# Kernel tuning notes

Measured on AMD Instinct MI355X. Metric: run time of the kernel, lower is better.

## Reference

```python
import jax, jax.numpy as jnp
import numpy as np

THRESH = 0.1  # Hardshrink lambda from init_kwargs


def setup_inputs() -> dict:
    key = jax.random.key(0)
    k1, k2, k3 = jax.random.split(key, 3)
    m, n, N = 64, 256, 131072
    phi = jax.random.normal(k1, (m, n), dtype=jnp.float32)
    X = jax.random.normal(k2, (n, N), dtype=jnp.float32)
    Y = jax.random.normal(k3, (m, N), dtype=jnp.float32)
    step = jnp.ones((1,), dtype=jnp.float32)  # learnable ISTA step size
    return {"phi": phi, "X": X, "Y": Y, "step": step, "idx": 100000}


def reference(phi, X, Y, step, idx):
    # The torch module updates column idx, then columns 0..idx-1, each with
    #   X[:, i] = hardshrink(X[:, i] + step * phi.T @ (Y[:, i] - phi @ X[:, i]))
    # (note: -(-1)*step == +step). Columns are independent and each column
    # reads only its own pre-update value, so the per-column loop is exactly
    # equivalent to two batched GEMMs over the prefix X[:, :idx+1] plus one
    # fused hard-threshold pass.
    k = idx + 1  # number of updated columns (idx is a static Python int)
    cols = X[:, :k]                       # [n, k]
    resid = Y[:, :k] - phi @ cols         # [m, k]
    upd = cols + step[0] * (phi.T @ resid)  # [n, k] gradient step
    upd = jnp.where(jnp.abs(upd) > THRESH, upd, jnp.zeros((), upd.dtype))
    X = X.at[:, :k].set(upd)
    return phi, X
```

## Files before the change

### kernel.cpp

```cpp
#include <hip/hip_runtime.h>
#include <math.h>

constexpr int M   = 64;
constexpr int NR  = 256;
constexpr int KK  = NR + M;
constexpr int NC  = 131072;
constexpr int BN  = 64;
constexpr float THR = 0.1f;

typedef __bf16 bf16x8 __attribute__((ext_vector_type(8)));
typedef float  f32x4  __attribute__((ext_vector_type(4)));

static __device__ __forceinline__ unsigned short f2bf(float f) {
    unsigned int u = __float_as_uint(f);
    u += 0x7FFFu + ((u >> 16) & 1u);
    return (unsigned short)(u >> 16);
}

__global__ __launch_bounds__(256)
void k_copy_phi(const float* __restrict__ phi, float* __restrict__ out)
{
    int i = blockIdx.x * 256 + threadIdx.x;
    out[i] = phi[i];
}

__global__ __launch_bounds__(256)
void k_prep(const float* __restrict__ phi, const float* __restrict__ step,
            unsigned short* __restrict__ A)
{
    __shared__ float ph[M * NR];
    const int i = blockIdx.x, j = threadIdx.x;
    for (int t = j; t < M * NR; t += 256) ph[t] = phi[t];
    __syncthreads();
    const float s = step[0];
    float d = 0.f;
    #pragma unroll
    for (int m = 0; m < M; ++m)
        d = fmaf(ph[m * NR + i], ph[m * NR + j], d);
    float w = ((i == j) ? 1.f : 0.f) - s * d;
    A[i * KK + j] = f2bf(w);
    if (j < M) A[i * KK + NR + j] = f2bf(s * ph[j * NR + i]);
}

__global__ __launch_bounds__(256, 3)
void k_gemm(const unsigned short* __restrict__ A,
            const float* __restrict__ X,
            const float* __restrict__ Y,
            const int*   __restrict__ idxp,
            float* __restrict__ outX)
{
    const int k   = idxp[0] + 1;
    const int n0  = blockIdx.x * BN;
    const int tid = threadIdx.x;

    if (n0 >= k) {
        const int c4 = tid & 15, rg = tid >> 4;
        #pragma unroll 4
        for (int r = rg; r < NR; r += 16) {
            const float4* src = (const float4*)(X + (size_t)r * NC + n0);
            float4*       dst = (float4*)(outX + (size_t)r * NC + n0);
            dst[c4] = src[c4];
        }
        return;
    }

    __shared__ unsigned int Bu32[10 * 2560 / 2];

    {
        const int n = tid & 63, slot = tid >> 6;
        for (int p = slot; p < KK / 2; p += 4) {
            const int r = p << 1;
            const float* s0 = (r < NR) ? (X + (size_t)r * NC)
                                       : (Y + (size_t)(r - NR) * NC);
            const float* s1 = (r < NR) ? (X + (size_t)(r + 1) * NC)
                                       : (Y + (size_t)(r + 1 - NR) * NC);
            float v0 = s0[n0 + n], v1 = s1[n0 + n];
            const int kb = r >> 5, kl = r & 31;
            Bu32[(kb * 2560 + n * 40 + kl) >> 1] =
                (unsigned int)f2bf(v0) | ((unsigned int)f2bf(v1) << 16);
        }
    }
    __syncthreads();

    const int lane = tid & 63, wave = tid >> 6;
    const int quad = lane >> 4, nlo = lane & 15;
    const int mbase = wave * 64;

    f32x4 acc[4][4];
    #pragma unroll
    for (int mt = 0; mt < 4; ++mt)
        #pragma unroll
        for (int nt = 0; nt < 4; ++nt)
            acc[mt][nt] = (f32x4){0.f, 0.f, 0.f, 0.f};

    const unsigned short* Abase = A + (size_t)(mbase + nlo) * KK + quad * 8;
    const unsigned int*   Bbase = Bu32 + ((nlo * 40 + quad * 8) >> 1);

    #pragma unroll 2
    for (int kb = 0; kb < 10; ++kb) {
        bf16x8 afr[4], bfr[4];
        #pragma unroll
        for (int mt = 0; mt < 4; ++mt)
            afr[mt] = *(const bf16x8*)(Abase + (size_t)mt * 16 * KK + kb * 32);
        #pragma unroll
        for (int nt = 0; nt < 4; ++nt)
            bfr[nt] = *(const bf16x8*)(Bbase + (kb * 2560 + nt * 16 * 40) / 2);
        #pragma unroll
        for (int mt = 0; mt < 4; ++mt)
            #pragma unroll
            for (int nt = 0; nt < 4; ++nt)
                acc[mt][nt] = __builtin_amdgcn_mfma_f32_16x16x32_bf16(
                    afr[mt], bfr[nt], acc[mt][nt], 0, 0, 0);
    }

    const bool boundary = (n0 + BN > k);
    #pragma unroll
    for (int mt = 0; mt < 4; ++mt) {
        #pragma unroll
        for (int nt = 0; nt < 4; ++nt) {
            const int col = n0 + nt * 16 + nlo;
            #pragma unroll
            for (int reg = 0; reg < 4; ++reg) {
                const int row = mbase + mt * 16 + quad * 4 + reg;
                float v = acc[mt][nt][reg];
                v = (fabsf(v) > THR) ? v : 0.f;
                if (boundary && col >= k) v = X[(size_t)row * NC + col];
                outX[(size_t)row * NC + col] = v;
            }
        }
    }
}

extern "C" void kernel_launch(void* const* d_in, const int* in_sizes, int n_in,
                              void* d_out, int out_size, void* d_ws, size_t ws_size,
                              hipStream_t stream)
{
    const float* phi  = (const float*)d_in[0];
    const float* X    = (const float*)d_in[1];
    const float* Y    = (const float*)d_in[2];
    const float* step = (const float*)d_in[3];
    const int*   idx  = (const int*)d_in[4];
    float* out = (float*)d_out;
    unsigned short* A = (unsigned short*)d_ws;

    k_copy_phi<<<(M * NR) / 256, 256, 0, stream>>>(phi, out);
    k_prep<<<NR, 256, 0, stream>>>(phi, step, A);
    k_gemm<<<NC / BN, 256, 0, stream>>>(A, X, Y, idx, out + M * NR);
}
```

Baseline: 323.8 us.

## Halve GEMM column tile, vectorize B staging, prefetch A fragments

Shrinks the per-block column tile from 64 to 32, doubling the grid and raising the occupancy hint to 4 blocks per CU. B staging now uses float2 loads with a cheaper round-half bf16 pack via byte permute, and a padded stride-17 LDS layout meant to avoid bank conflicts. A fragments are software-prefetched one k-step ahead in registers. The intent is more parallelism and better latency hiding on this memory-bound kernel, at the cost of reloading A twice as often and a slightly different bf16 rounding (ties no longer go to even).

```diff
diff --git a/kernel.cpp b/kernel.cpp
--- a/kernel.cpp
+++ b/kernel.cpp
@@ -5,16 +5,28 @@
 constexpr int NR  = 256;
 constexpr int KK  = NR + M;
 constexpr int NC  = 131072;
-constexpr int BN  = 64;
+constexpr int BN  = 32;
+constexpr int NT  = BN / 16;
+constexpr int KB  = KK / 32;
 constexpr float THR = 0.1f;
+
+constexpr int LDS_U32 = KB * 544;
 
 typedef __bf16 bf16x8 __attribute__((ext_vector_type(8)));
 typedef float  f32x4  __attribute__((ext_vector_type(4)));
+
+union U4BF8 { uint4 u; bf16x8 v; };
 
 static __device__ __forceinline__ unsigned short f2bf(float f) {
     unsigned int u = __float_as_uint(f);
     u += 0x7FFFu + ((u >> 16) & 1u);
     return (unsigned short)(u >> 16);
+}
+
+static __device__ __forceinline__ unsigned int pack_rh(float a, float b) {
+    unsigned int ua = __float_as_uint(a) + 0x8000u;
+    unsigned int ub = __float_as_uint(b) + 0x8000u;
+    return __builtin_amdgcn_perm(ua, ub, 0x03020706u);
 }
 
 __global__ __launch_bounds__(256)
@@ -42,89 +54,109 @@
     if (j < M) A[i * KK + NR + j] = f2bf(s * ph[j * NR + i]);
 }
 
-__global__ __launch_bounds__(256, 3)
+__global__ __launch_bounds__(256, 4)
 void k_gemm(const unsigned short* __restrict__ A,
             const float* __restrict__ X,
             const float* __restrict__ Y,
             const int*   __restrict__ idxp,
             float* __restrict__ outX)
 {
-    const int k   = idxp[0] + 1;
-    const int n0  = blockIdx.x * BN;
-    const int tid = threadIdx.x;
+    const int kcols = idxp[0] + 1;
+    const int n0    = blockIdx.x * BN;
+    const int tid   = threadIdx.x;
 
-    if (n0 >= k) {
-        const int c4 = tid & 15, rg = tid >> 4;
-        #pragma unroll 4
-        for (int r = rg; r < NR; r += 16) {
+    if (n0 >= kcols) {
+        const int c8 = tid & 7, rg = tid >> 3;
+        #pragma unroll
+        for (int r = rg; r < NR; r += 32) {
             const float4* src = (const float4*)(X + (size_t)r * NC + n0);
             float4*       dst = (float4*)(outX + (size_t)r * NC + n0);
-            dst[c4] = src[c4];
+            dst[c8] = src[c8];
         }
         return;
     }
-
-    __shared__ unsigned int Bu32[10 * 2560 / 2];
-
-    {
-        const int n = tid & 63, slot = tid >> 6;
-        for (int p = slot; p < KK / 2; p += 4) {
-            const int r = p << 1;
-            const float* s0 = (r < NR) ? (X + (size_t)r * NC)
-                                       : (Y + (size_t)(r - NR) * NC);
-            const float* s1 = (r < NR) ? (X + (size_t)(r + 1) * NC)
-                                       : (Y + (size_t)(r + 1 - NR) * NC);
-            float v0 = s0[n0 + n], v1 = s1[n0 + n];
-            const int kb = r >> 5, kl = r & 31;
-            Bu32[(kb * 2560 + n * 40 + kl) >> 1] =
-                (unsigned int)f2bf(v0) | ((unsigned int)f2bf(v1) << 16);
-        }
-    }
-    __syncthreads();
 
     const int lane = tid & 63, wave = tid >> 6;
     const int quad = lane >> 4, nlo = lane & 15;
     const int mbase = wave * 64;
 
-    f32x4 acc[4][4];
+    const unsigned short* Ab = A + (size_t)(mbase + nlo) * KK + quad * 8;
+    bf16x8 a_cur[4];
+    #pragma unroll
+    for (int mt = 0; mt < 4; ++mt)
+        a_cur[mt] = *(const bf16x8*)(Ab + (size_t)mt * 16 * KK);
+
+    __shared__ unsigned int B[LDS_U32];
+
+    {
+        const int ng  = tid & 15;
+        const int rp0 = tid >> 4;
+        #pragma unroll
+        for (int it = 0; it < 10; ++it) {
+            const int rp = rp0 + 16 * it;
+            const int r  = rp << 1;
+            const float* b0 = (r < NR) ? (X + (size_t)r * NC)
+                                       : (Y + (size_t)(r - NR) * NC);
+            const float* b1 = (r < NR) ? (X + (size_t)(r + 1) * NC)
+                                       : (Y + (size_t)(r + 1 - NR) * NC);
+            float2 v0 = ((const float2*)(b0 + n0))[ng];
+            float2 v1 = ((const float2*)(b1 + n0))[ng];
+            const int base = (r >> 5) * 544 + ((r & 31) >> 1);
+            B[base + (2 * ng)     * 17] = pack_rh(v0.x, v1.x);
+            B[base + (2 * ng + 1) * 17] = pack_rh(v0.y, v1.y);
+        }
+    }
+    __syncthreads();
+
+    f32x4 acc[4][NT];
     #pragma unroll
     for (int mt = 0; mt < 4; ++mt)
         #pragma unroll
-        for (int nt = 0; nt < 4; ++nt)
+        for (int nt = 0; nt < NT; ++nt)
             acc[mt][nt] = (f32x4){0.f, 0.f, 0.f, 0.f};
 
-    const unsigned short* Abase = A + (size_t)(mbase + nlo) * KK + quad * 8;
-    const unsigned int*   Bbase = Bu32 + ((nlo * 40 + quad * 8) >> 1);
+    const unsigned int* Bb = B + nlo * 17 + quad * 4;
 
-    #pragma unroll 2
-    for (int kb = 0; kb < 10; ++kb) {
-        bf16x8 afr[4], bfr[4];
+    #pragma unroll
+    for (int kb = 0; kb < KB; ++kb) {
+        bf16x8 a_nxt[4];
+        if (kb < KB - 1) {
+            #pragma unroll
+            for (int mt = 0; mt < 4; ++mt)
+                a_nxt[mt] = *(const bf16x8*)(Ab + (size_t)mt * 16 * KK + (kb + 1) * 32);
+        }
+        bf16x8 bfr[NT];
         #pragma unroll
-        for (int mt = 0; mt < 4; ++mt)
-            afr[mt] = *(const bf16x8*)(Abase + (size_t)mt * 16 * KK + kb * 32);
-        #pragma unroll
-        for (int nt = 0; nt < 4; ++nt)
-            bfr[nt] = *(const bf16x8*)(Bbase + (kb * 2560 + nt * 16 * 40) / 2);
+        for (int nt = 0; nt < NT; ++nt) {
+            const unsigned int* p = Bb + kb * 544 + nt * 272;
+            U4BF8 t;
+            t.u.x = p[0]; t.u.y = p[1]; t.u.z = p[2]; t.u.w = p[3];
+            bfr[nt] = t.v;
+        }
         #pragma unroll
         for (int mt = 0; mt < 4; ++mt)
             #pragma unroll
-            for (int nt = 0; nt < 4; ++nt)
+            for (int nt = 0; nt < NT; ++nt)
                 acc[mt][nt] = __builtin_amdgcn_mfma_f32_16x16x32_bf16(
-                    afr[mt], bfr[nt], acc[mt][nt], 0, 0, 0);
+                    a_cur[mt], bfr[nt], acc[mt][nt], 0, 0, 0);
+        if (kb < KB - 1) {
+            #pragma unroll
+            for (int mt = 0; mt < 4; ++mt) a_cur[mt] = a_nxt[mt];
+        }
     }
 
-    const bool boundary = (n0 + BN > k);
+    const bool boundary = (n0 + BN > kcols);
     #pragma unroll
     for (int mt = 0; mt < 4; ++mt) {
         #pragma unroll
-        for (int nt = 0; nt < 4; ++nt) {
+        for (int nt = 0; nt < NT; ++nt) {
             const int col = n0 + nt * 16 + nlo;
             #pragma unroll
             for (int reg = 0; reg < 4; ++reg) {
                 const int row = mbase + mt * 16 + quad * 4 + reg;
                 float v = acc[mt][nt][reg];
                 v = (fabsf(v) > THR) ? v : 0.f;
-                if (boundary && col >= k) v = X[(size_t)row * NC + col];
+                if (boundary && col >= kcols) v = X[(size_t)row * NC + col];
                 outX[(size_t)row * NC + col] = v;
             }
         }
```

Result: slower. 335.3 us (+3.5%).
